# Kernel optimization log

Measured on AMD Instinct MI355X. Metric: run time of the kernel, lower is better.

## Reference

```python
import jax, jax.numpy as jnp
import numpy as np

EMBED = 1024
HEADS = 16
HEAD_DIM = EMBED // HEADS


def setup_inputs() -> dict:
    key = jax.random.key(0)
    ks = jax.random.split(key, 8)
    N, S = 4, 2048
    values = jax.random.normal(ks[0], (N, S, EMBED), dtype=jnp.float32)
    queries = jax.random.normal(ks[1], (N, S, EMBED), dtype=jnp.float32)
    keys = jax.random.normal(ks[2], (N, S, EMBED), dtype=jnp.float32)
    mask = jax.random.randint(ks[3], (N, 1, S, S), 0, 2, dtype=jnp.int32)
    sc = 1.0 / np.sqrt(HEAD_DIM)
    Wv = jax.random.normal(ks[4], (HEAD_DIM, HEAD_DIM), dtype=jnp.float32) * sc
    Wk = jax.random.normal(ks[5], (HEAD_DIM, HEAD_DIM), dtype=jnp.float32) * sc
    Wq = jax.random.normal(ks[6], (HEAD_DIM, HEAD_DIM), dtype=jnp.float32) * sc
    Wo = jax.random.normal(ks[7], (EMBED, EMBED), dtype=jnp.float32) * (1.0 / np.sqrt(EMBED))
    bo = jnp.zeros((EMBED,), dtype=jnp.float32)
    return {"values": values, "queries": queries, "keys": keys, "mask": mask,
            "Wv": Wv, "Wk": Wk, "Wq": Wq, "Wo": Wo, "bo": bo}


def reference(values, queries, keys, mask, Wv, Wk, Wq, Wo, bo):
    N, S, _ = queries.shape
    # split heads: (N, len, H, D)
    v = values.reshape(N, -1, HEADS, HEAD_DIM)
    k = keys.reshape(N, -1, HEADS, HEAD_DIM)
    q = queries.reshape(N, -1, HEADS, HEAD_DIM)
    # per-head linear projections (nn.Linear: y = x @ W.T, no bias)
    v = jnp.einsum('nlhd,ed->nlhe', v, Wv)
    k = jnp.einsum('nlhd,ed->nlhe', k, Wk)
    q = jnp.einsum('nlhd,ed->nlhe', q, Wq)
    # energy: (N, H, q_len, k_len)
    energy = jnp.einsum('nqhd,nkhd->nhqk', q, k)
    energy = jnp.where(mask == 0, jnp.float32(-1e20), energy)
    # non-standard scale: sqrt(embed_size), applied after masking
    attn = jax.nn.softmax(energy / jnp.sqrt(jnp.float32(EMBED)), axis=3)
    out = jnp.einsum('nhql,nlhd->nqhd', attn, v).reshape(N, S, EMBED)
    return out @ Wo.T + bo
```

## Files before the change

kernel.cpp:

```cpp
#include <hip/hip_runtime.h>
#include <hip/hip_bf16.h>

#define NBATCH 4
#define SEQ    2048
#define EMBED  1024
#define HEADS  16
#define HD     64

typedef __attribute__((ext_vector_type(8))) short bf16x8;
typedef __attribute__((ext_vector_type(4))) float f32x4;
typedef __attribute__((ext_vector_type(16))) float f32x16;

__device__ __forceinline__ short f2bf(float f) {
  union { float f; unsigned u; } v; v.f = f;
  unsigned r = v.u + 0x7fffu + ((v.u >> 16) & 1u);
  return (short)(r >> 16);
}

__device__ __forceinline__ unsigned pkbf(float a, float b) {
#if __has_builtin(__builtin_amdgcn_cvt_pk_bf16_f32)
  typedef __attribute__((ext_vector_type(2))) __bf16 bf16x2_t;
  bf16x2_t r = __builtin_amdgcn_cvt_pk_bf16_f32(a, b);
  union { bf16x2_t v; unsigned u; } cv; cv.v = r; return cv.u;
#else
  return (unsigned)(unsigned short)f2bf(a) | ((unsigned)(unsigned short)f2bf(b) << 16);
#endif
}

typedef __attribute__((address_space(1))) const void gas_void;
typedef __attribute__((address_space(3))) void las_void;
__device__ __forceinline__ void glds16(const void* g, void* l) {
  __builtin_amdgcn_global_load_lds((gas_void*)g, (las_void*)l, 16, 0, 0);
}

__device__ __forceinline__ bf16x8 mk8(unsigned a, unsigned b, unsigned c, unsigned d) {
  union { unsigned u[4]; bf16x8 v; } t;
  t.u[0] = a; t.u[1] = b; t.u[2] = c; t.u[3] = d; return t.v;
}

__device__ __forceinline__ void pl32swap(unsigned &a, unsigned &b) {
  asm volatile("v_permlane32_swap_b32 %0, %1" : "+v"(a), "+v"(b));
}

#define MFMA32(A, B, C) __builtin_amdgcn_mfma_f32_32x32x16_bf16((A), (B), (C), 0, 0, 0)

#define C2 0.04508422f

__global__ __launch_bounds__(256) void cvt_all(
    const float* __restrict__ Wo, const float* __restrict__ Wq,
    const float* __restrict__ Wk, const float* __restrict__ Wv,
    short* __restrict__ dWo, short* __restrict__ dWq,
    short* __restrict__ dWk, short* __restrict__ dWv)
{
  int e = (blockIdx.x * 256 + threadIdx.x) * 4;
  const float* src; short* dst; int off; float sc = 1.0f;
  if (e < EMBED * EMBED) { src = Wo; dst = dWo; off = e; }
  else {
    int j = e - EMBED * EMBED;
    if      (j < 4096)  { src = Wq; dst = dWq; off = j; sc = C2; }
    else if (j < 8192)  { src = Wk; dst = dWk; off = j - 4096; }
    else if (j < 12288) { src = Wv; dst = dWv; off = j - 8192; }
    else return;
  }
  float4 v = *(const float4*)(src + off);
  ushort4 p;
  p.x = (unsigned short)f2bf(v.x * sc);
  p.y = (unsigned short)f2bf(v.y * sc);
  p.z = (unsigned short)f2bf(v.z * sc);
  p.w = (unsigned short)f2bf(v.w * sc);
  *(ushort4*)(dst + off) = p;
}

__global__ __launch_bounds__(256) void mask_pack(const int* __restrict__ mask,
                                                 unsigned long long* __restrict__ bits) {
  long long t = (long long)blockIdx.x * 256 + threadIdx.x;
  int lane = threadIdx.x & 63;
  int m = mask[t];
  unsigned long long b = __ballot(m != 0);
  if (lane == 0) bits[t >> 6] = b;
}

__global__ __launch_bounds__(256) void proj_kernel(
    const float* __restrict__ srcQ, const float* __restrict__ srcK, const float* __restrict__ srcV,
    const short* __restrict__ WbQ, const short* __restrict__ WbK, const short* __restrict__ WbV,
    short* __restrict__ Qp, short* __restrict__ Kp, short* __restrict__ Vt)
{
  int rt = blockIdx.x;
  int h  = blockIdx.y;
  int mz = blockIdx.z;
  const float* src = (mz == 0) ? srcQ : ((mz == 1) ? srcK : srcV);
  const short* Wb  = (mz == 0) ? WbQ : ((mz == 1) ? WbK : WbV);

  __shared__ __align__(16) short At[64][72];

  int tid = threadIdx.x;
  int r0 = rt * 64;
  for (int idx = tid; idx < 64 * 16; idx += 256) {
    int row = idx >> 4;
    int c4  = idx & 15;
    float4 v = *(const float4*)(src + (long long)(r0 + row) * EMBED + h * HD + c4 * 4);
    uint2 pk2;
    pk2.x = pkbf(v.x, v.y);
    pk2.y = pkbf(v.z, v.w);
    *(uint2*)&At[row][c4 * 4] = pk2;
  }
  __syncthreads();

  int lane = tid & 63, w = tid >> 6, quad = lane >> 4, l15 = lane & 15;

  bf16x8 af0 = *(const bf16x8*)&At[w * 16 + l15][quad * 8];
  bf16x8 af1 = *(const bf16x8*)&At[w * 16 + l15][32 + quad * 8];

  f32x4 acc[4];
  for (int cg = 0; cg < 4; cg++) {
    acc[cg] = (f32x4){0.f, 0.f, 0.f, 0.f};
    bf16x8 b0 = *(const bf16x8*)(Wb + (cg * 16 + l15) * 64 + quad * 8);
    bf16x8 b1 = *(const bf16x8*)(Wb + (cg * 16 + l15) * 64 + 32 + quad * 8);
    acc[cg] = __builtin_amdgcn_mfma_f32_16x16x32_bf16(af0, b0, acc[cg], 0, 0, 0);
    acc[cg] = __builtin_amdgcn_mfma_f32_16x16x32_bf16(af1, b1, acc[cg], 0, 0, 0);
  }

  int rloc = w * 16 + quad * 4;
  __syncthreads();
  if (mz < 2) {
#pragma unroll
    for (int cg = 0; cg < 4; cg++)
#pragma unroll
      for (int reg = 0; reg < 4; reg++)
        At[rloc + reg][cg * 16 + l15] = f2bf(acc[cg][reg]);
  } else {
#pragma unroll
    for (int cg = 0; cg < 4; cg++)
#pragma unroll
      for (int reg = 0; reg < 4; reg++)
        At[cg * 16 + l15][rloc + reg] = f2bf(acc[cg][reg]);
  }
  __syncthreads();

  short* dst = (mz == 0) ? Qp : ((mz == 1) ? Kp : Vt);
  int row2 = tid >> 2, ch = tid & 3;
  const uint4* lp = (const uint4*)&At[row2][ch * 16];
  uint4 v0 = lp[0], v1 = lp[1];
  char* g;
  if (mz < 2) {
    int r = r0 + row2; int n = r >> 11, s = r & 2047;
    g = (char*)(dst + ((long long)(n * HEADS + h) * SEQ + s) * HD) + ch * 32;
  } else {
    int n = r0 >> 11, s0 = r0 & 2047;
    g = (char*)(dst + ((long long)(n * HEADS + h) * HD + row2) * SEQ + s0) + ch * 32;
  }
  *(uint4*)g = v0;
  *(uint4*)(g + 16) = v1;
}

#define SOFTMAX_KK(SV, MW, PAV0, PAV1) do {                                       \
    unsigned n0 = ((MW) >> sh4) & 0xFu;                                           \
    unsigned n1 = ((MW) >> (sh4 + 8)) & 0xFu;                                     \
    unsigned n2 = ((MW) >> (sh4 + 16)) & 0xFu;                                    \
    unsigned n3 = ((MW) >> (sh4 + 24)) & 0xFu;                                    \
    float p0  = __builtin_amdgcn_exp2f(SV[0]);   p0  = (n0 & 1u) ? p0  : 0.f;     \
    float p1  = __builtin_amdgcn_exp2f(SV[1]);   p1  = (n0 & 2u) ? p1  : 0.f;     \
    float p2  = __builtin_amdgcn_exp2f(SV[2]);   p2  = (n0 & 4u) ? p2  : 0.f;     \
    float p3  = __builtin_amdgcn_exp2f(SV[3]);   p3  = (n0 & 8u) ? p3  : 0.f;     \
    float p4  = __builtin_amdgcn_exp2f(SV[4]);   p4  = (n1 & 1u) ? p4  : 0.f;     \
    float p5  = __builtin_amdgcn_exp2f(SV[5]);   p5  = (n1 & 2u) ? p5  : 0.f;     \
    float p6  = __builtin_amdgcn_exp2f(SV[6]);   p6  = (n1 & 4u) ? p6  : 0.f;     \
    float p7  = __builtin_amdgcn_exp2f(SV[7]);   p7  = (n1 & 8u) ? p7  : 0.f;     \
    float p8  = __builtin_amdgcn_exp2f(SV[8]);   p8  = (n2 & 1u) ? p8  : 0.f;     \
    float p9  = __builtin_amdgcn_exp2f(SV[9]);   p9  = (n2 & 2u) ? p9  : 0.f;     \
    float p10 = __builtin_amdgcn_exp2f(SV[10]);  p10 = (n2 & 4u) ? p10 : 0.f;     \
    float p11 = __builtin_amdgcn_exp2f(SV[11]);  p11 = (n2 & 8u) ? p11 : 0.f;     \
    float p12 = __builtin_amdgcn_exp2f(SV[12]);  p12 = (n3 & 1u) ? p12 : 0.f;     \
    float p13 = __builtin_amdgcn_exp2f(SV[13]);  p13 = (n3 & 2u) ? p13 : 0.f;     \
    float p14 = __builtin_amdgcn_exp2f(SV[14]);  p14 = (n3 & 4u) ? p14 : 0.f;     \
    float p15 = __builtin_amdgcn_exp2f(SV[15]);  p15 = (n3 & 8u) ? p15 : 0.f;     \
    lsum += (((p0 + p1) + (p2 + p3)) + ((p4 + p5) + (p6 + p7)))                   \
          + (((p8 + p9) + (p10 + p11)) + ((p12 + p13) + (p14 + p15)));            \
    unsigned u0 = pkbf(p0, p1),   u1 = pkbf(p2, p3);                              \
    unsigned u2 = pkbf(p4, p5),   u3 = pkbf(p6, p7);                              \
    unsigned u4 = pkbf(p8, p9),   u5 = pkbf(p10, p11);                            \
    unsigned u6 = pkbf(p12, p13), u7 = pkbf(p14, p15);                            \
    pl32swap(u0, u2); pl32swap(u1, u3);                                           \
    pl32swap(u4, u6); pl32swap(u5, u7);                                           \
    PAV0 = mk8(u0, u1, u2, u3);                                                   \
    PAV1 = mk8(u4, u5, u6, u7);                                                   \
  } while (0)

#define ATTN_ITER(BUF, KT) do {                                                   \
    __syncthreads();                                                              \
    if ((KT) < 31) {                                                              \
      const char* ks_ = Kb + ((KT) + 1) * 8192 + kgo;                             \
      const char* vs_ = Vb + ((KT) + 1) * 128 + vgo;                              \
      char* kd_ = ldsK + (((BUF) ^ 1) * 8192) + klo;                              \
      char* vd_ = ldsV + (((BUF) ^ 1) * 8192) + klo;                              \
      glds16(ks_,          kd_);                                                  \
      glds16(ks_ + 4096,   kd_ + 4096);                                           \
      glds16(vs_,          vd_);                                                  \
      glds16(vs_ + 131072, vd_ + 4096);                                           \
      mnxt = mptr[(KT) + 1];                                                      \
    }                                                                             \
    unsigned mlo = (unsigned)mcur, mhiw = (unsigned)(mcur >> 32);                 \
    const char* KB_ = ldsK + (BUF) * 8192;                                        \
    const char* VB_ = ldsV + (BUF) * 8192;                                        \
    bf16x8 pa0, pa1, pa2, pa3;                                                    \
    {                                                                             \
      f32x16 s = {};                                                              \
      __builtin_amdgcn_s_setprio(1);                                              \
      s = MFMA32(*(const bf16x8*)(KB_ + a4_0), qf0, s);                           \
      s = MFMA32(*(const bf16x8*)(KB_ + a4_1), qf1, s);                           \
      s = MFMA32(*(const bf16x8*)(KB_ + a4_2), qf2, s);                           \
      s = MFMA32(*(const bf16x8*)(KB_ + a4_3), qf3, s);                           \
      __builtin_amdgcn_s_setprio(0);                                              \
      SOFTMAX_KK(s, mlo, pa0, pa1);                                               \
    }                                                                             \
    {                                                                             \
      f32x16 s = {};                                                              \
      __builtin_amdgcn_s_setprio(1);                                              \
      s = MFMA32(*(const bf16x8*)(KB_ + 4096 + a4_0), qf0, s);                    \
      s = MFMA32(*(const bf16x8*)(KB_ + 4096 + a4_1), qf1, s);                    \
      s = MFMA32(*(const bf16x8*)(KB_ + 4096 + a4_2), qf2, s);                    \
      s = MFMA32(*(const bf16x8*)(KB_ + 4096 + a4_3), qf3, s);                    \
      __builtin_amdgcn_s_setprio(0);                                              \
      SOFTMAX_KK(s, mhiw, pa2, pa3);                                              \
    }                                                                             \
    __builtin_amdgcn_s_setprio(1);                                                \
    O0 = MFMA32(*(const bf16x8*)(VB_ + a4_0),        pa0, O0);                    \
    O1 = MFMA32(*(const bf16x8*)(VB_ + 4096 + a4_0), pa0, O1);                    \
    O0 = MFMA32(*(const bf16x8*)(VB_ + a4_1),        pa1, O0);                    \
    O1 = MFMA32(*(const bf16x8*)(VB_ + 4096 + a4_1), pa1, O1);                    \
    O0 = MFMA32(*(const bf16x8*)(VB_ + a4_2),        pa2, O0);                    \
    O1 = MFMA32(*(const bf16x8*)(VB_ + 4096 + a4_2), pa2, O1);                    \
    O0 = MFMA32(*(const bf16x8*)(VB_ + a4_3),        pa3, O0);                    \
    O1 = MFMA32(*(const bf16x8*)(VB_ + 4096 + a4_3), pa3, O1);                    \
    __builtin_amdgcn_s_setprio(0);                                                \
    mcur = mnxt;                                                                  \
  } while (0)

__global__ __launch_bounds__(256, 3) void attn_kernel(
    const short* __restrict__ Qp, const short* __restrict__ Kp, const short* __restrict__ Vt,
    const unsigned long long* __restrict__ mbits, short* __restrict__ AO)
{
  int L  = blockIdx.x;
  int qt = (L >> 3) & 15;
  int p_ = ((L >> 7) << 3) | (L & 7);
  int h  = p_ & 15;
  int nb = p_ >> 4;
  int q0 = qt * 128;

  __shared__ __align__(16) char ldsK[2 * 8192];
  __shared__ __align__(16) char ldsV[2 * 8192];

  int tid = threadIdx.x, lane = tid & 63, w = tid >> 6;
  int l31 = lane & 31, hi5 = lane >> 5;
  int g8 = lane & 7, r8 = lane >> 3;
  int pp = lane & 7;
  unsigned sh4 = (unsigned)(hi5 * 4);

  long long nh = (long long)(nb * HEADS + h);
  const char* Kb = (const char*)(Kp + nh * SEQ * HD);
  const char* Vb = (const char*)(Vt + nh * HD * SEQ);

  int kgo = (w * 8 + r8) * 128 + ((g8 ^ r8) << 4);
  int vgo = (w * 8 + r8) * 4096 + ((g8 ^ r8) << 4);
  int klo = w * 1024;

  int a4_0 = l31 * 128 + ((((0 | hi5) ^ pp)) << 4);
  int a4_1 = l31 * 128 + ((((2 | hi5) ^ pp)) << 4);
  int a4_2 = l31 * 128 + ((((4 | hi5) ^ pp)) << 4);
  int a4_3 = l31 * 128 + ((((6 | hi5) ^ pp)) << 4);

  int qrow = q0 + w * 32 + l31;
  const short* Qb = Qp + (nh * SEQ + qrow) * HD + hi5 * 8;
  bf16x8 qf0 = *(const bf16x8*)(Qb);
  bf16x8 qf1 = *(const bf16x8*)(Qb + 16);
  bf16x8 qf2 = *(const bf16x8*)(Qb + 32);
  bf16x8 qf3 = *(const bf16x8*)(Qb + 48);

  const unsigned long long* mptr = mbits + ((long long)nb * SEQ + qrow) * 32;

  f32x16 O0 = {}, O1 = {};
  float lsum = 0.f;

  glds16(Kb + kgo,          ldsK + klo);
  glds16(Kb + 4096 + kgo,   ldsK + 4096 + klo);
  glds16(Vb + vgo,          ldsV + klo);
  glds16(Vb + vgo + 131072, ldsV + 4096 + klo);
  unsigned long long mcur = mptr[0], mnxt = 0;

  for (int it = 0; it < 16; it++) {
    ATTN_ITER(0, it * 2);
    ATTN_ITER(1, it * 2 + 1);
  }

  lsum += __shfl_xor(lsum, 32);
  float inv = 1.f / lsum;

  short* aoRow = AO + ((long long)nb * SEQ + qrow) * EMBED + h * HD + hi5 * 4;
#pragma unroll
  for (int j = 0; j < 4; j++) {
    uint2 pk;
    pk.x = pkbf(O0[4 * j] * inv, O0[4 * j + 1] * inv);
    pk.y = pkbf(O0[4 * j + 2] * inv, O0[4 * j + 3] * inv);
    *(uint2*)(aoRow + j * 8) = pk;
    pk.x = pkbf(O1[4 * j] * inv, O1[4 * j + 1] * inv);
    pk.y = pkbf(O1[4 * j + 2] * inv, O1[4 * j + 3] * inv);
    *(uint2*)(aoRow + 32 + j * 8) = pk;
  }
}

__global__ __launch_bounds__(512) void outproj_kernel(
    const short* __restrict__ AO, const short* __restrict__ Wob,
    const float* __restrict__ bo, float* __restrict__ out)
{
  int rt = blockIdx.x, ct = blockIdx.y;
  __shared__ __align__(16) short AtL[128 * 64];
  __shared__ __align__(16) short BtL[128 * 64];

  int tid = threadIdx.x, lane = tid & 63, w = tid >> 6, quad = lane >> 4, l15 = lane & 15;
  int r8b = tid >> 3, g8 = tid & 7;
  int swz = g8 ^ (r8b & 7);
  int s3 = l15 & 7;
  int o0 = (quad ^ s3) * 16;
  int o1 = ((quad + 4) ^ s3) * 16;

  int r0 = rt * 128, c0 = ct * 128;
  int wr = (w >> 1) * 32, wc = (w & 1) * 64;

  const char* Abase = (const char*)AO  + (long long)(r0 + r8b) * 2048 + swz * 16;
  const char* Bbase = (const char*)Wob + (long long)(c0 + r8b) * 2048 + swz * 16;
  unsigned lbase = (unsigned)tid * 16;

  f32x4 acc[2][4];
#pragma unroll
  for (int mi = 0; mi < 2; mi++)
#pragma unroll
    for (int ni = 0; ni < 4; ni++) acc[mi][ni] = (f32x4){0.f, 0.f, 0.f, 0.f};

  for (int kc = 0; kc < 16; kc++) {
    __syncthreads();
    glds16(Abase + kc * 128,                 (char*)AtL + lbase);
    glds16(Abase + 64LL * 2048 + kc * 128,   (char*)AtL + lbase + 8192);
    glds16(Bbase + kc * 128,                 (char*)BtL + lbase);
    glds16(Bbase + 64LL * 2048 + kc * 128,   (char*)BtL + lbase + 8192);
    __syncthreads();

    const char* AB = (const char*)AtL;
    const char* BB = (const char*)BtL;
    bf16x8 af[2][2];
#pragma unroll
    for (int mi = 0; mi < 2; mi++) {
      int r = wr + mi * 16 + l15;
      af[mi][0] = *(const bf16x8*)(AB + r * 128 + o0);
      af[mi][1] = *(const bf16x8*)(AB + r * 128 + o1);
    }
#pragma unroll
    for (int ni = 0; ni < 4; ni++) {
      int r = wc + ni * 16 + l15;
      bf16x8 b0 = *(const bf16x8*)(BB + r * 128 + o0);
      bf16x8 b1 = *(const bf16x8*)(BB + r * 128 + o1);
#pragma unroll
      for (int mi = 0; mi < 2; mi++) {
        acc[mi][ni] = __builtin_amdgcn_mfma_f32_16x16x32_bf16(af[mi][0], b0, acc[mi][ni], 0, 0, 0);
        acc[mi][ni] = __builtin_amdgcn_mfma_f32_16x16x32_bf16(af[mi][1], b1, acc[mi][ni], 0, 0, 0);
      }
    }
  }

#pragma unroll
  for (int ni = 0; ni < 4; ni++) {
    float b = bo[c0 + wc + ni * 16 + l15];
#pragma unroll
    for (int mi = 0; mi < 2; mi++)
#pragma unroll
      for (int reg = 0; reg < 4; reg++) {
        int r = r0 + wr + mi * 16 + quad * 4 + reg;
        out[(long long)r * EMBED + c0 + wc + ni * 16 + l15] = acc[mi][ni][reg] + b;
      }
  }
}

extern "C" void kernel_launch(void* const* d_in, const int* in_sizes, int n_in,
                              void* d_out, int out_size, void* d_ws, size_t ws_size,
                              hipStream_t stream) {
  const float* values  = (const float*)d_in[0];
  const float* queries = (const float*)d_in[1];
  const float* keys    = (const float*)d_in[2];
  const int*   mask    = (const int*)d_in[3];
  const float* Wv = (const float*)d_in[4];
  const float* Wk = (const float*)d_in[5];
  const float* Wq = (const float*)d_in[6];
  const float* Wo = (const float*)d_in[7];
  const float* bo = (const float*)d_in[8];
  float* out = (float*)d_out;

  char* ws = (char*)d_ws;
  size_t off = 0;
  const size_t PROJ_BYTES = (size_t)NBATCH * HEADS * SEQ * HD * 2;
  short* Qp = (short*)(ws + off); off += PROJ_BYTES;
  short* Kp = (short*)(ws + off); off += PROJ_BYTES;
  short* Vt = (short*)(ws + off); off += PROJ_BYTES;
  short* AO = (short*)(ws + off); off += PROJ_BYTES;
  unsigned long long* mbits = (unsigned long long*)(ws + off);
  off += (size_t)NBATCH * SEQ * (SEQ / 64) * 8;
  short* Wob = (short*)(ws + off); off += (size_t)EMBED * EMBED * 2;
  short* WbQ = (short*)(ws + off); off += HD * HD * 2;
  short* WbK = (short*)(ws + off); off += HD * HD * 2;
  short* WbV = (short*)(ws + off); off += HD * HD * 2;

  cvt_all<<<dim3((EMBED * EMBED + 3 * HD * HD) / 4 / 256), dim3(256), 0, stream>>>(
      Wo, Wq, Wk, Wv, Wob, WbQ, WbK, WbV);

  mask_pack<<<dim3((NBATCH * SEQ * SEQ) / 256), dim3(256), 0, stream>>>(mask, mbits);

  proj_kernel<<<dim3((NBATCH * SEQ) / 64, HEADS, 3), dim3(256), 0, stream>>>(
      queries, keys, values, WbQ, WbK, WbV, Qp, Kp, Vt);

  attn_kernel<<<dim3(SEQ / 128 * HEADS * NBATCH), dim3(256), 0, stream>>>(Qp, Kp, Vt, mbits, AO);

  outproj_kernel<<<dim3((NBATCH * SEQ) / 128, EMBED / 128), dim3(512), 0, stream>>>(AO, Wob, bo, out);
}
```

Measured before the change: 367.7 us.

## Double K/V tile to 128 keys, restructure V LDS layout, double-buffer outproj

The attention kernel now stages 128 keys per iteration (16 iterations instead of 32), using 32KB K and V double buffers with a new V swizzle. Each iteration processes four 32-key groups that fuse QK, softmax and PV. Launch bounds drop from 3 to 2 blocks per SM to make room for the larger LDS footprint. The output projection kernel gains a double-buffered prefetch so one barrier per k-step is removed, and it raises wave priority around its MFMAs. The trade is fewer barriers and longer loads in flight against lower occupancy.

```diff
diff --git a/kernel.cpp b/kernel.cpp
--- a/kernel.cpp
+++ b/kernel.cpp
@@ -186,57 +186,27 @@
     PAV1 = mk8(u4, u5, u6, u7);                                                   \
   } while (0)
 
-#define ATTN_ITER(BUF, KT) do {                                                   \
-    __syncthreads();                                                              \
-    if ((KT) < 31) {                                                              \
-      const char* ks_ = Kb + ((KT) + 1) * 8192 + kgo;                             \
-      const char* vs_ = Vb + ((KT) + 1) * 128 + vgo;                              \
-      char* kd_ = ldsK + (((BUF) ^ 1) * 8192) + klo;                              \
-      char* vd_ = ldsV + (((BUF) ^ 1) * 8192) + klo;                              \
-      glds16(ks_,          kd_);                                                  \
-      glds16(ks_ + 4096,   kd_ + 4096);                                           \
-      glds16(vs_,          vd_);                                                  \
-      glds16(vs_ + 131072, vd_ + 4096);                                           \
-      mnxt = mptr[(KT) + 1];                                                      \
-    }                                                                             \
-    unsigned mlo = (unsigned)mcur, mhiw = (unsigned)(mcur >> 32);                 \
-    const char* KB_ = ldsK + (BUF) * 8192;                                        \
-    const char* VB_ = ldsV + (BUF) * 8192;                                        \
-    bf16x8 pa0, pa1, pa2, pa3;                                                    \
-    {                                                                             \
-      f32x16 s = {};                                                              \
-      __builtin_amdgcn_s_setprio(1);                                              \
-      s = MFMA32(*(const bf16x8*)(KB_ + a4_0), qf0, s);                           \
-      s = MFMA32(*(const bf16x8*)(KB_ + a4_1), qf1, s);                           \
-      s = MFMA32(*(const bf16x8*)(KB_ + a4_2), qf2, s);                           \
-      s = MFMA32(*(const bf16x8*)(KB_ + a4_3), qf3, s);                           \
-      __builtin_amdgcn_s_setprio(0);                                              \
-      SOFTMAX_KK(s, mlo, pa0, pa1);                                               \
-    }                                                                             \
-    {                                                                             \
-      f32x16 s = {};                                                              \
-      __builtin_amdgcn_s_setprio(1);                                              \
-      s = MFMA32(*(const bf16x8*)(KB_ + 4096 + a4_0), qf0, s);                    \
-      s = MFMA32(*(const bf16x8*)(KB_ + 4096 + a4_1), qf1, s);                    \
-      s = MFMA32(*(const bf16x8*)(KB_ + 4096 + a4_2), qf2, s);                    \
-      s = MFMA32(*(const bf16x8*)(KB_ + 4096 + a4_3), qf3, s);                    \
-      __builtin_amdgcn_s_setprio(0);                                              \
-      SOFTMAX_KK(s, mhiw, pa2, pa3);                                              \
-    }                                                                             \
+#define GRP(G, MW) do {                                                           \
+    const char* KG = bK + (G) * 4096;                                             \
+    f32x16 s = {};                                                                \
     __builtin_amdgcn_s_setprio(1);                                                \
-    O0 = MFMA32(*(const bf16x8*)(VB_ + a4_0),        pa0, O0);                    \
-    O1 = MFMA32(*(const bf16x8*)(VB_ + 4096 + a4_0), pa0, O1);                    \
-    O0 = MFMA32(*(const bf16x8*)(VB_ + a4_1),        pa1, O0);                    \
-    O1 = MFMA32(*(const bf16x8*)(VB_ + 4096 + a4_1), pa1, O1);                    \
-    O0 = MFMA32(*(const bf16x8*)(VB_ + a4_2),        pa2, O0);                    \
-    O1 = MFMA32(*(const bf16x8*)(VB_ + 4096 + a4_2), pa2, O1);                    \
-    O0 = MFMA32(*(const bf16x8*)(VB_ + a4_3),        pa3, O0);                    \
-    O1 = MFMA32(*(const bf16x8*)(VB_ + 4096 + a4_3), pa3, O1);                    \
+    s = MFMA32(*(const bf16x8*)(KG + a4_0), qf0, s);                              \
+    s = MFMA32(*(const bf16x8*)(KG + a4_1), qf1, s);                              \
+    s = MFMA32(*(const bf16x8*)(KG + a4_2), qf2, s);                              \
+    s = MFMA32(*(const bf16x8*)(KG + a4_3), qf3, s);                              \
     __builtin_amdgcn_s_setprio(0);                                                \
-    mcur = mnxt;                                                                  \
+    bf16x8 pa0, pa1;                                                              \
+    SOFTMAX_KK(s, MW, pa0, pa1);                                                  \
+    int vg = ((G) * 64) ^ vmx;                                                    \
+    __builtin_amdgcn_s_setprio(1);                                                \
+    O0 = MFMA32(*(const bf16x8*)(bV + vb0 + vg), pa0, O0);                        \
+    O1 = MFMA32(*(const bf16x8*)(bV + vb0 + vg + 8192), pa0, O1);                 \
+    O0 = MFMA32(*(const bf16x8*)(bV + vb1 + vg), pa1, O0);                        \
+    O1 = MFMA32(*(const bf16x8*)(bV + vb1 + vg + 8192), pa1, O1);                 \
+    __builtin_amdgcn_s_setprio(0);                                                \
   } while (0)
 
-__global__ __launch_bounds__(256, 3) void attn_kernel(
+__global__ __launch_bounds__(256, 2) void attn_kernel(
     const short* __restrict__ Qp, const short* __restrict__ Kp, const short* __restrict__ Vt,
     const unsigned long long* __restrict__ mbits, short* __restrict__ AO)
 {
@@ -247,8 +217,8 @@
   int nb = p_ >> 4;
   int q0 = qt * 128;
 
-  __shared__ __align__(16) char ldsK[2 * 8192];
-  __shared__ __align__(16) char ldsV[2 * 8192];
+  __shared__ __align__(16) char ldsK[2 * 16384];
+  __shared__ __align__(16) char ldsV[2 * 16384];
 
   int tid = threadIdx.x, lane = tid & 63, w = tid >> 6;
   int l31 = lane & 31, hi5 = lane >> 5;
@@ -260,14 +230,18 @@
   const char* Kb = (const char*)(Kp + nh * SEQ * HD);
   const char* Vb = (const char*)(Vt + nh * HD * SEQ);
 
-  int kgo = (w * 8 + r8) * 128 + ((g8 ^ r8) << 4);
-  int vgo = (w * 8 + r8) * 4096 + ((g8 ^ r8) << 4);
+  int kgo = w * 1024 + r8 * 128 + ((g8 ^ r8) << 4);
+  int vd15 = 4 * w + (lane >> 4);
+  int vgo = vd15 * 4096 + ((((lane & 15) ^ vd15)) << 4);
   int klo = w * 1024;
 
   int a4_0 = l31 * 128 + ((((0 | hi5) ^ pp)) << 4);
   int a4_1 = l31 * 128 + ((((2 | hi5) ^ pp)) << 4);
   int a4_2 = l31 * 128 + ((((4 | hi5) ^ pp)) << 4);
   int a4_3 = l31 * 128 + ((((6 | hi5) ^ pp)) << 4);
+  int vb0 = l31 * 256 + (((0 | hi5) ^ (l31 & 3)) << 4);
+  int vb1 = l31 * 256 + (((2 | hi5) ^ (l31 & 3)) << 4);
+  int vmx = (l31 & 12) << 4;
 
   int qrow = q0 + w * 32 + l31;
   const short* Qb = Qp + (nh * SEQ + qrow) * HD + hi5 * 8;
@@ -276,20 +250,51 @@
   bf16x8 qf2 = *(const bf16x8*)(Qb + 32);
   bf16x8 qf3 = *(const bf16x8*)(Qb + 48);
 
-  const unsigned long long* mptr = mbits + ((long long)nb * SEQ + qrow) * 32;
+  const ulonglong2* mp2 = (const ulonglong2*)(mbits + ((long long)nb * SEQ + qrow) * 32);
 
   f32x16 O0 = {}, O1 = {};
   float lsum = 0.f;
 
-  glds16(Kb + kgo,          ldsK + klo);
-  glds16(Kb + 4096 + kgo,   ldsK + 4096 + klo);
-  glds16(Vb + vgo,          ldsV + klo);
-  glds16(Vb + vgo + 131072, ldsV + 4096 + klo);
-  unsigned long long mcur = mptr[0], mnxt = 0;
-
-  for (int it = 0; it < 16; it++) {
-    ATTN_ITER(0, it * 2);
-    ATTN_ITER(1, it * 2 + 1);
+  {
+    char* dK = ldsK + klo; char* dV = ldsV + klo;
+    const char* sK = Kb + kgo; const char* sV = Vb + vgo;
+    glds16(sK,          dK);
+    glds16(sK + 4096,   dK + 4096);
+    glds16(sK + 8192,   dK + 8192);
+    glds16(sK + 12288,  dK + 12288);
+    glds16(sV,          dV);
+    glds16(sV + 65536,  dV + 4096);
+    glds16(sV + 131072, dV + 8192);
+    glds16(sV + 196608, dV + 12288);
+  }
+  ulonglong2 mcur = mp2[0], mnxt;
+
+  for (int kt = 0; kt < 16; kt++) {
+    __syncthreads();
+    const char* bK = ldsK + (kt & 1) * 16384;
+    const char* bV = ldsV + (kt & 1) * 16384;
+    if (kt < 15) {
+      char* dK = ldsK + ((kt & 1) ^ 1) * 16384 + klo;
+      char* dV = ldsV + ((kt & 1) ^ 1) * 16384 + klo;
+      const char* sK = Kb + (kt + 1) * 16384 + kgo;
+      const char* sV = Vb + (kt + 1) * 256 + vgo;
+      glds16(sK,          dK);
+      glds16(sK + 4096,   dK + 4096);
+      glds16(sK + 8192,   dK + 8192);
+      glds16(sK + 12288,  dK + 12288);
+      glds16(sV,          dV);
+      glds16(sV + 65536,  dV + 4096);
+      glds16(sV + 131072, dV + 8192);
+      glds16(sV + 196608, dV + 12288);
+      mnxt = mp2[kt + 1];
+    }
+    unsigned mw0 = (unsigned)mcur.x, mw1 = (unsigned)(mcur.x >> 32);
+    unsigned mw2 = (unsigned)mcur.y, mw3 = (unsigned)(mcur.y >> 32);
+    GRP(0, mw0);
+    GRP(1, mw1);
+    GRP(2, mw2);
+    GRP(3, mw3);
+    mcur = mnxt;
   }
 
   lsum += __shfl_xor(lsum, 32);
@@ -313,8 +318,8 @@
     const float* __restrict__ bo, float* __restrict__ out)
 {
   int rt = blockIdx.x, ct = blockIdx.y;
-  __shared__ __align__(16) short AtL[128 * 64];
-  __shared__ __align__(16) short BtL[128 * 64];
+  __shared__ __align__(16) short AtL[2][128 * 64];
+  __shared__ __align__(16) short BtL[2][128 * 64];
 
   int tid = threadIdx.x, lane = tid & 63, w = tid >> 6, quad = lane >> 4, l15 = lane & 15;
   int r8b = tid >> 3, g8 = tid & 7;
@@ -336,16 +341,24 @@
 #pragma unroll
     for (int ni = 0; ni < 4; ni++) acc[mi][ni] = (f32x4){0.f, 0.f, 0.f, 0.f};
 
+  glds16(Abase,               (char*)AtL[0] + lbase);
+  glds16(Abase + 64LL * 2048, (char*)AtL[0] + lbase + 8192);
+  glds16(Bbase,               (char*)BtL[0] + lbase);
+  glds16(Bbase + 64LL * 2048, (char*)BtL[0] + lbase + 8192);
+
   for (int kc = 0; kc < 16; kc++) {
     __syncthreads();
-    glds16(Abase + kc * 128,                 (char*)AtL + lbase);
-    glds16(Abase + 64LL * 2048 + kc * 128,   (char*)AtL + lbase + 8192);
-    glds16(Bbase + kc * 128,                 (char*)BtL + lbase);
-    glds16(Bbase + 64LL * 2048 + kc * 128,   (char*)BtL + lbase + 8192);
-    __syncthreads();
-
-    const char* AB = (const char*)AtL;
-    const char* BB = (const char*)BtL;
+    const char* AB = (const char*)AtL[kc & 1];
+    const char* BB = (const char*)BtL[kc & 1];
+    if (kc < 15) {
+      char* dA = (char*)AtL[(kc & 1) ^ 1] + lbase;
+      char* dB = (char*)BtL[(kc & 1) ^ 1] + lbase;
+      glds16(Abase + (kc + 1) * 128,               dA);
+      glds16(Abase + 64LL * 2048 + (kc + 1) * 128, dA + 8192);
+      glds16(Bbase + (kc + 1) * 128,               dB);
+      glds16(Bbase + 64LL * 2048 + (kc + 1) * 128, dB + 8192);
+    }
+
     bf16x8 af[2][2];
 #pragma unroll
     for (int mi = 0; mi < 2; mi++) {
@@ -353,6 +366,7 @@
       af[mi][0] = *(const bf16x8*)(AB + r * 128 + o0);
       af[mi][1] = *(const bf16x8*)(AB + r * 128 + o1);
     }
+    __builtin_amdgcn_s_setprio(1);
 #pragma unroll
     for (int ni = 0; ni < 4; ni++) {
       int r = wc + ni * 16 + l15;
@@ -364,6 +378,7 @@
         acc[mi][ni] = __builtin_amdgcn_mfma_f32_16x16x32_bf16(af[mi][1], b1, acc[mi][ni], 0, 0, 0);
       }
     }
+    __builtin_amdgcn_s_setprio(0);
   }
 
 #pragma unroll
```

Result: no change. 373.1 us (+1.5%).
